# Kernel optimization log

Measured on AMD Instinct MI355X. Metric: run time of the kernel, lower is better.

Reference implementation:

```python
import jax, jax.numpy as jnp
import numpy as np

B, T, D, H = 2, 1024, 1024, 16
HS = D // H
EPS = 1e-5
SCALE = float(np.sqrt(HS))  # faithful bug: scores / hs**(-0.5) == scores * sqrt(hs)


def setup_inputs() -> dict:
    key = jax.random.key(0)
    ks = jax.random.split(key, 20)
    n = lambda k, shape: jax.random.normal(k, shape, dtype=jnp.float32) * 0.02
    return {
        "src": jax.random.normal(ks[0], (B, T, D), dtype=jnp.float32),
        "att": jax.random.normal(ks[1], (B, T, D), dtype=jnp.float32),
        # causal masked self-attention (no biases on q/k/v)
        "wq_m": n(ks[2], (H, D, HS)), "wk_m": n(ks[3], (H, D, HS)), "wv_m": n(ks[4], (H, D, HS)),
        "proj_m_w": n(ks[5], (D, D)), "proj_m_b": jnp.zeros((D,), jnp.float32),
        # final (cross) attention (biases on q/k/v)
        "wq_f": n(ks[6], (H, D, HS)), "wk_f": n(ks[7], (H, D, HS)), "wv_f": n(ks[8], (H, D, HS)),
        "bq_f": jnp.zeros((H, HS), jnp.float32), "bk_f": jnp.zeros((H, HS), jnp.float32),
        "bv_f": jnp.zeros((H, HS), jnp.float32),
        "proj_f_w": n(ks[9], (D, D)), "proj_f_b": jnp.zeros((D,), jnp.float32),
        # FFN
        "w1": n(ks[10], (D, 4 * D)), "b1": jnp.zeros((4 * D,), jnp.float32),
        "w2": n(ks[11], (4 * D, D)), "b2": jnp.zeros((D,), jnp.float32),
        # shared RMSNorm weight (one instance reused at all three sites)
        "norm_w": jnp.ones((D,), jnp.float32),
    }


def rmsnorm(x, w):
    return x * jax.lax.rsqrt(jnp.mean(x * x, axis=-1, keepdims=True) + EPS) * w


def masked_attn(x, wq, wk, wv):
    q = jnp.einsum('btd,hde->bhte', x, wq)
    k = jnp.einsum('btd,hde->bhte', x, wk)
    v = jnp.einsum('btd,hde->bhte', x, wv)
    scores = jnp.einsum('bhte,bhse->bhts', q, k) * SCALE  # [B,H,T,T]
    causal = jnp.tril(jnp.ones((T, T), dtype=bool))
    scores = jnp.where(causal, scores, -jnp.inf)
    a = jax.nn.softmax(scores, axis=-1)
    o = jnp.einsum('bhts,bhse->bhte', a, v)
    return o.transpose(0, 2, 1, 3).reshape(B, T, D)  # concat heads


def final_attn(x, att, wq, bq, wk, bk, wv, bv):
    q = jnp.einsum('btd,hde->bhte', att, wq) + bq[None, :, None, :]
    k = jnp.einsum('btd,hde->bhte', att, wk) + bk[None, :, None, :]
    v = jnp.einsum('btd,hde->bhte', x, wv) + bv[None, :, None, :]
    scores = jnp.einsum('bhte,bhse->bhts', q, k) * SCALE
    a = jax.nn.softmax(scores, axis=-1)
    o = jnp.einsum('bhts,bhse->bhte', a, v)
    return o.transpose(0, 2, 1, 3).reshape(B, T, D)


def reference(src, att, wq_m, wk_m, wv_m, proj_m_w, proj_m_b,
              wq_f, wk_f, wv_f, bq_f, bk_f, bv_f, proj_f_w, proj_f_b,
              w1, b1, w2, b2, norm_w):
    # masked self-attention block
    m = masked_attn(rmsnorm(src, norm_w), wq_m, wk_m, wv_m)
    m_out = src + (m @ proj_m_w + proj_m_b)
    # cross attention block (q/k from norm(att), v from m_out)
    f = final_attn(m_out, rmsnorm(att, norm_w), wq_f, bq_f, wk_f, bk_f, wv_f, bv_f)
    f_out = m_out + (f @ proj_f_w + proj_f_b)
    # FFN block
    h = rmsnorm(f_out, norm_w)
    h = jax.nn.gelu(h @ w1 + b1, approximate=False) @ w2 + b2
    return f_out + h
```

## Files before the change

### kernel.cpp

```cpp
#include <hip/hip_runtime.h>
#include <math.h>

#define BB 2
#define TT 1024
#define DD 1024
#define HH 16
#define HS 64
#define NROWS (BB*TT)

typedef _Float16 f16;
typedef __attribute__((ext_vector_type(8))) _Float16 half8;
typedef __attribute__((ext_vector_type(4))) _Float16 half4;
typedef __attribute__((ext_vector_type(4))) float f32x4;

constexpr float EPS   = 1e-5f;
constexpr float SCALE = 8.0f;

__device__ __forceinline__ void load_lds16(const f16* g, f16* l) {
    __builtin_amdgcn_global_load_lds(
        (const __attribute__((address_space(1))) unsigned int*)g,
        (__attribute__((address_space(3))) unsigned int*)l, 16, 0, 0);
}

__device__ __forceinline__ int xcd_swizzle(int lin, int total) {
    if ((total & 7) == 0) {
        const int chunk = total >> 3;
        lin = (lin & 7) * chunk + (lin >> 3);
    }
    return lin;
}

__global__ __launch_bounds__(256) void rmsnorm_kernel(const float* __restrict__ x,
                                                      const float* __restrict__ w,
                                                      f16* __restrict__ out) {
    const int row = blockIdx.x;
    const int tid = threadIdx.x;
    const float* xr = x + (size_t)row * DD;

    float4 xv = reinterpret_cast<const float4*>(xr)[tid];
    float ss = xv.x*xv.x + xv.y*xv.y + xv.z*xv.z + xv.w*xv.w;

    __shared__ float red[256];
    red[tid] = ss; __syncthreads();
    for (int s = 128; s > 0; s >>= 1) {
        if (tid < s) red[tid] += red[tid + s];
        __syncthreads();
    }
    const float inv = rsqrtf(red[0] * (1.0f / DD) + EPS);

    float4 wv = reinterpret_cast<const float4*>(w)[tid];
    half4 o;
    o.x = (f16)(xv.x * inv * wv.x);
    o.y = (f16)(xv.y * inv * wv.y);
    o.z = (f16)(xv.z * inv * wv.z);
    o.w = (f16)(xv.w * inv * wv.w);
    *reinterpret_cast<half4*>(&out[(size_t)row * DD + tid * 4]) = o;
}

template<bool HEADW>
__global__ __launch_bounds__(256) void wtrans(const float* __restrict__ W,
                                              f16* __restrict__ Wt,
                                              int K, int N) {
    __shared__ float t[64][65];
    const int k0 = blockIdx.x * 64;
    const int n0 = blockIdx.y * 64;
    const int tid = threadIdx.x;

    #pragma unroll
    for (int r = 0; r < 4; ++r) {
        const int idx = tid + r * 256;
        const int kl  = idx >> 4;
        const int nl4 = (idx & 15) * 4;
        const float* gp;
        if (HEADW) {
            gp = W + ((size_t)(n0 >> 6) * K + (k0 + kl)) * 64 + nl4;
        } else {
            gp = W + (size_t)(k0 + kl) * N + n0 + nl4;
        }
        float4 v = *reinterpret_cast<const float4*>(gp);
        t[kl][nl4 + 0] = v.x; t[kl][nl4 + 1] = v.y;
        t[kl][nl4 + 2] = v.z; t[kl][nl4 + 3] = v.w;
    }
    __syncthreads();
    #pragma unroll
    for (int r = 0; r < 4; ++r) {
        const int idx = tid + r * 256;
        const int nl  = idx >> 4;
        const int kl4 = (idx & 15) * 4;
        half4 o;
        o.x = (f16)t[kl4 + 0][nl];
        o.y = (f16)t[kl4 + 1][nl];
        o.z = (f16)t[kl4 + 2][nl];
        o.w = (f16)t[kl4 + 3][nl];
        *reinterpret_cast<half4*>(&Wt[(size_t)(n0 + nl) * K + k0 + kl4]) = o;
    }
}

__global__ void pack_bias(const float* __restrict__ a, const float* __restrict__ b,
                          const float* __restrict__ c, float* __restrict__ o) {
    const int i = blockIdx.x * 256 + threadIdx.x;
    if (i < 1024) { o[i] = a[i]; o[i + 1024] = b[i]; o[i + 2048] = c[i]; }
}

template<int BM, int EPI, bool HEADOUT, bool SPLITA, bool OHALF, bool OUT2, bool PARTIAL>
__global__ __launch_bounds__(256, 2) void gemm_mfma(
    const f16* __restrict__ A1,
    const f16* __restrict__ A2,
    const f16* __restrict__ Bt,
    const float* __restrict__ bias,
    const float* __restrict__ resid,
    float* __restrict__ outF,
    f16* __restrict__ outH,
    f16* __restrict__ outH2,
    int N, int K, int splitN)
{
    constexpr int BK = 32;
    constexpr int MI = 4;
    constexpr int NI = (BM == 128) ? 4 : 2;
    constexpr int WN = (BM == 128) ? 64 : 32;
    constexpr int ASLOT = BM * 4;
    constexpr int AINST = ASLOT / 256;

    __shared__ f16 ldsA[2][ASLOT * 8];
    __shared__ f16 ldsB[2][512 * 8];

    const int tid  = threadIdx.x;
    const int lane = tid & 63;
    const int wid  = tid >> 6;
    const int gx = gridDim.x;
    const int lin = xcd_swizzle(blockIdx.y * gx + blockIdx.x, gx * gridDim.y);
    const int m0 = (lin / gx) * BM;
    const int n0 = (lin % gx) * 128;
    const int wm = (BM == 128) ? (wid >> 1) : 0;
    const int wn = (BM == 128) ? (wid & 1) : wid;

    const int Klen  = K / gridDim.z;
    const int kbase = blockIdx.z * Klen;

    const f16* Aptr = (SPLITA && n0 >= splitN) ? A2 : A1;

    f32x4 acc[MI][NI];
    #pragma unroll
    for (int i = 0; i < MI; ++i)
        #pragma unroll
        for (int j = 0; j < NI; ++j)
            acc[i][j] = (f32x4){0.f, 0.f, 0.f, 0.f};

    auto stage = [&](int buf, int kt) {
        const int k0 = kbase + kt * BK;
        #pragma unroll
        for (int i = 0; i < AINST; ++i) {
            const int s   = (wid * AINST + i) * 64 + lane;
            const int kh  = s / BM;
            const int row = s % BM;
            load_lds16(Aptr + (size_t)(m0 + row) * K + (k0 + kh * 8),
                       &ldsA[buf][s * 8]);
        }
        #pragma unroll
        for (int i = 0; i < 2; ++i) {
            const int s   = (wid * 2 + i) * 64 + lane;
            const int kh  = s >> 7;
            const int col = s & 127;
            load_lds16(Bt + (size_t)(n0 + col) * K + (k0 + kh * 8),
                       &ldsB[buf][s * 8]);
        }
    };

    const int NT = Klen / BK;
    stage(0, 0);
    __syncthreads();
    int cur = 0;
    const int l15 = lane & 15, l4 = lane >> 4;
    for (int kt = 0; kt < NT; ++kt) {
        if (kt + 1 < NT) stage(cur ^ 1, kt + 1);
        half8 af[MI], bfr[NI];
        #pragma unroll
        for (int mi = 0; mi < MI; ++mi)
            af[mi] = *reinterpret_cast<const half8*>(
                &ldsA[cur][(l4 * BM + wm * 64 + mi * 16 + l15) * 8]);
        #pragma unroll
        for (int ni = 0; ni < NI; ++ni)
            bfr[ni] = *reinterpret_cast<const half8*>(
                &ldsB[cur][(l4 * 128 + wn * WN + ni * 16 + l15) * 8]);
        #pragma unroll
        for (int mi = 0; mi < MI; ++mi)
            #pragma unroll
            for (int ni = 0; ni < NI; ++ni)
                acc[mi][ni] = __builtin_amdgcn_mfma_f32_16x16x32_f16(
                    af[mi], bfr[ni], acc[mi][ni], 0, 0, 0);
        __syncthreads();
        cur ^= 1;
    }

    float* pout = nullptr;
    if (PARTIAL) {
        const size_t MN = (size_t)gridDim.y * BM * N;
        pout = outF + (size_t)blockIdx.z * MN;
    }

    #pragma unroll
    for (int mi = 0; mi < MI; ++mi) {
        #pragma unroll
        for (int ni = 0; ni < NI; ++ni) {
            #pragma unroll
            for (int r = 0; r < 4; ++r) {
                const int row = m0 + wm * 64 + mi * 16 + l4 * 4 + r;
                const int col = n0 + wn * WN + ni * 16 + l15;
                float v = acc[mi][ni][r];
                if (PARTIAL) {
                    pout[(size_t)row * N + col] = v;
                    continue;
                }
                if (EPI >= 1) v += bias[col];
                if (EPI == 2) v = 0.5f * v * (1.0f + erff(v * 0.70710678118f));
                if (EPI == 3) v += resid[(size_t)row * N + col];
                size_t oidx;
                if (HEADOUT) {
                    const int mat = col >> 10;
                    const int h = (col >> 6) & 15, e = col & 63;
                    const int b = row >> 10, t = row & (TT - 1);
                    oidx = (size_t)mat * ((size_t)NROWS * DD)
                         + ((size_t)((b * HH + h) * TT + t)) * HS + e;
                } else {
                    oidx = (size_t)row * N + col;
                }
                if (OHALF) outH[oidx] = (f16)v;
                else       outF[oidx] = v;
                if (OUT2)  outH2[oidx] = (f16)v;
            }
        }
    }
}

template<bool OUT2>
__global__ __launch_bounds__(256) void reduce4(const float* __restrict__ part,
                                               const float* __restrict__ bias,
                                               const float* __restrict__ resid,
                                               float* __restrict__ outF,
                                               f16* __restrict__ outH2,
                                               int N) {
    const size_t MN  = (size_t)gridDim.x * 1024;
    const size_t idx = ((size_t)blockIdx.x * 256 + threadIdx.x) * 4;
    float4 a = *reinterpret_cast<const float4*>(part + idx);
    float4 b = *reinterpret_cast<const float4*>(part + MN + idx);
    float4 c = *reinterpret_cast<const float4*>(part + 2 * MN + idx);
    float4 d = *reinterpret_cast<const float4*>(part + 3 * MN + idx);
    float4 bi = *reinterpret_cast<const float4*>(bias + (idx & (size_t)(N - 1)));
    float4 rs = *reinterpret_cast<const float4*>(resid + idx);
    float4 o;
    o.x = a.x + b.x + c.x + d.x + bi.x + rs.x;
    o.y = a.y + b.y + c.y + d.y + bi.y + rs.y;
    o.z = a.z + b.z + c.z + d.z + bi.z + rs.z;
    o.w = a.w + b.w + c.w + d.w + bi.w + rs.w;
    *reinterpret_cast<float4*>(outF + idx) = o;
    if (OUT2) {
        half4 h;
        h.x = (f16)o.x; h.y = (f16)o.y; h.z = (f16)o.z; h.w = (f16)o.w;
        *reinterpret_cast<half4*>(outH2 + idx) = h;
    }
}

template<bool CAUSAL>
__global__ __launch_bounds__(256) void attn_mfma(const f16* __restrict__ Q,
                                                 const f16* __restrict__ Kg,
                                                 const f16* __restrict__ Vg,
                                                 f16* __restrict__ O) {
    const int iq  = blockIdx.x;
    const int bh  = blockIdx.y;
    const int tid = threadIdx.x;
    const int lane = tid & 63;
    const int w   = tid >> 6;
    const int l15 = lane & 15, l4 = lane >> 4;

    __shared__ f16 Ks[512 * 8];
    __shared__ f16 VT[64 * 72];
    __shared__ f16 Ps[4][16 * 72];

    const f16* qb = Q  + ((size_t)bh * TT + (size_t)iq * 64) * HS;
    const f16* kb = Kg + (size_t)bh * TT * HS;
    const f16* vb = Vg + (size_t)bh * TT * HS;

    half8 qf[2];
    #pragma unroll
    for (int ks = 0; ks < 2; ++ks)
        qf[ks] = *reinterpret_cast<const half8*>(
            qb + (size_t)(w * 16 + l15) * HS + ks * 32 + l4 * 8);

    f32x4 oacc[4];
    #pragma unroll
    for (int ni = 0; ni < 4; ++ni) oacc[ni] = (f32x4){0.f, 0.f, 0.f, 0.f};
    float m_run[4], l_run[4];
    #pragma unroll
    for (int r = 0; r < 4; ++r) { m_run[r] = -1e30f; l_run[r] = 0.f; }

    const int sp  = lane & 31;
    const int ehv = lane >> 5;
    const int c0  = w * 16 + ehv * 8;

    const int ntiles = CAUSAL ? (iq + 1) : (TT / 64);
    for (int js = 0; js < ntiles; ++js) {
        __syncthreads();

        #pragma unroll
        for (int i = 0; i < 2; ++i) {
            const int slot = (w * 2 + i) * 64 + lane;
            load_lds16(kb + (size_t)(js * 64 + (slot & 63)) * HS + (slot >> 6) * 8,
                       &Ks[slot * 8]);
        }
        {
            const f16* vrow = vb + (size_t)(js * 64 + 2 * sp) * HS + c0;
            uint4 r0 = *reinterpret_cast<const uint4*>(vrow);
            uint4 r1 = *reinterpret_cast<const uint4*>(vrow + HS);
            const unsigned rc0[4] = {r0.x, r0.y, r0.z, r0.w};
            const unsigned rc1[4] = {r1.x, r1.y, r1.z, r1.w};
            #pragma unroll
            for (int i = 0; i < 8; ++i) {
                const unsigned lo = (i & 1) ? (rc0[i >> 1] >> 16) : (rc0[i >> 1] & 0xffffu);
                const unsigned hi = (i & 1) ? (rc1[i >> 1] >> 16) : (rc1[i >> 1] & 0xffffu);
                *reinterpret_cast<unsigned*>(&VT[(c0 + i) * 72 + 2 * sp]) = lo | (hi << 16);
            }
        }
        __syncthreads();

        f32x4 sacc[4];
        #pragma unroll
        for (int ni = 0; ni < 4; ++ni) sacc[ni] = (f32x4){0.f, 0.f, 0.f, 0.f};
        #pragma unroll
        for (int ks = 0; ks < 2; ++ks) {
            #pragma unroll
            for (int ni = 0; ni < 4; ++ni) {
                half8 kf = *reinterpret_cast<const half8*>(
                    &Ks[((ks * 4 + l4) * 64 + ni * 16 + l15) * 8]);
                sacc[ni] = __builtin_amdgcn_mfma_f32_16x16x32_f16(qf[ks], kf, sacc[ni], 0, 0, 0);
            }
        }

        float sv[4][4];
        #pragma unroll
        for (int ni = 0; ni < 4; ++ni) {
            #pragma unroll
            for (int r = 0; r < 4; ++r) {
                float x = sacc[ni][r] * SCALE;
                if (CAUSAL && js == iq) {
                    const int sg = js * 64 + ni * 16 + l15;
                    const int qg = iq * 64 + w * 16 + l4 * 4 + r;
                    if (sg > qg) x = -1e30f;
                }
                sv[ni][r] = x;
            }
        }

        #pragma unroll
        for (int r = 0; r < 4; ++r) {
            float rm = fmaxf(fmaxf(sv[0][r], sv[1][r]), fmaxf(sv[2][r], sv[3][r]));
            rm = fmaxf(rm, __shfl_xor(rm, 1));
            rm = fmaxf(rm, __shfl_xor(rm, 2));
            rm = fmaxf(rm, __shfl_xor(rm, 4));
            rm = fmaxf(rm, __shfl_xor(rm, 8));
            const float mnew = fmaxf(m_run[r], rm);
            const float corr = __expf(m_run[r] - mnew);
            float p0 = __expf(sv[0][r] - mnew);
            float p1 = __expf(sv[1][r] - mnew);
            float p2 = __expf(sv[2][r] - mnew);
            float p3 = __expf(sv[3][r] - mnew);
            float sum = p0 + p1 + p2 + p3;
            sum += __shfl_xor(sum, 1);
            sum += __shfl_xor(sum, 2);
            sum += __shfl_xor(sum, 4);
            sum += __shfl_xor(sum, 8);
            l_run[r] = l_run[r] * corr + sum;
            m_run[r] = mnew;
            #pragma unroll
            for (int ni = 0; ni < 4; ++ni) oacc[ni][r] *= corr;
            f16* prow = &Ps[w][(l4 * 4 + r) * 72];
            prow[ 0 + l15] = (f16)p0;
            prow[16 + l15] = (f16)p1;
            prow[32 + l15] = (f16)p2;
            prow[48 + l15] = (f16)p3;
        }

        #pragma unroll
        for (int ks = 0; ks < 2; ++ks) {
            half8 pf = *reinterpret_cast<const half8*>(&Ps[w][l15 * 72 + ks * 32 + l4 * 8]);
            #pragma unroll
            for (int ni = 0; ni < 4; ++ni) {
                half8 vf = *reinterpret_cast<const half8*>(
                    &VT[(ni * 16 + l15) * 72 + ks * 32 + l4 * 8]);
                oacc[ni] = __builtin_amdgcn_mfma_f32_16x16x32_f16(pf, vf, oacc[ni], 0, 0, 0);
            }
        }
    }

    const int b = bh >> 4, h = bh & (HH - 1);
    #pragma unroll
    for (int r = 0; r < 4; ++r) {
        const float inv = 1.0f / l_run[r];
        const int t = iq * 64 + w * 16 + l4 * 4 + r;
        #pragma unroll
        for (int ni = 0; ni < 4; ++ni)
            O[((size_t)(b * TT + t)) * DD + h * HS + ni * 16 + l15] =
                (f16)(oacc[ni][r] * inv);
    }
}

extern "C" void kernel_launch(void* const* d_in, const int* in_sizes, int n_in,
                              void* d_out, int out_size, void* d_ws, size_t ws_size,
                              hipStream_t stream) {
    const float* src      = (const float*)d_in[0];
    const float* att      = (const float*)d_in[1];
    const float* wq_m     = (const float*)d_in[2];
    const float* wk_m     = (const float*)d_in[3];
    const float* wv_m     = (const float*)d_in[4];
    const float* proj_m_w = (const float*)d_in[5];
    const float* proj_m_b = (const float*)d_in[6];
    const float* wq_f     = (const float*)d_in[7];
    const float* wk_f     = (const float*)d_in[8];
    const float* wv_f     = (const float*)d_in[9];
    const float* bq_f     = (const float*)d_in[10];
    const float* bk_f     = (const float*)d_in[11];
    const float* bv_f     = (const float*)d_in[12];
    const float* proj_f_w = (const float*)d_in[13];
    const float* proj_f_b = (const float*)d_in[14];
    const float* w1       = (const float*)d_in[15];
    const float* b1       = (const float*)d_in[16];
    const float* w2       = (const float*)d_in[17];
    const float* b2       = (const float*)d_in[18];
    const float* norm_w   = (const float*)d_in[19];

    const size_t M_ = 1024 * 1024;
    f16* wsb = (f16*)d_ws;
    f16* wt_qkvm = wsb;
    f16* wt_projm = wsb + 3 * M_;
    f16* wt_qkvf = wsb + 4 * M_;
    f16* wt_projf = wsb + 7 * M_;
    f16* wt_w1   = wsb + 8 * M_;
    f16* wt_w2   = wsb + 12 * M_;
    f16* xn  = wsb + 16 * M_;
    f16* qkv = wsb + 18 * M_;
    f16* ao  = wsb + 24 * M_;
    f16* h1  = wsb + 18 * M_;
    float* m_out = (float*)(wsb + 26 * M_);
    float* partb = (float*)(wsb + 30 * M_);
    f16* mo_h  = (f16*)d_out;
    float* biascat = (float*)((char*)d_out + 4 * 1024 * 1024);
    float* f_out = (float*)d_out;
    float* outp  = (float*)d_out;
    (void)ws_size; (void)in_sizes; (void)n_in;

    const dim3 blk(256);
    const int BIG = 1 << 30;
    const dim3 gSPLIT(8, 16, 4);
    const dim3 gRED(2048);

    pack_bias<<<dim3(4), blk, 0, stream>>>(bq_f, bk_f, bv_f, biascat);
    wtrans<true ><<<dim3(16, 16), blk, 0, stream>>>(wq_m, wt_qkvm + 0 * M_, 1024, 1024);
    wtrans<true ><<<dim3(16, 16), blk, 0, stream>>>(wk_m, wt_qkvm + 1 * M_, 1024, 1024);
    wtrans<true ><<<dim3(16, 16), blk, 0, stream>>>(wv_m, wt_qkvm + 2 * M_, 1024, 1024);
    wtrans<false><<<dim3(16, 16), blk, 0, stream>>>(proj_m_w, wt_projm, 1024, 1024);
    wtrans<true ><<<dim3(16, 16), blk, 0, stream>>>(wq_f, wt_qkvf + 0 * M_, 1024, 1024);
    wtrans<true ><<<dim3(16, 16), blk, 0, stream>>>(wk_f, wt_qkvf + 1 * M_, 1024, 1024);
    wtrans<true ><<<dim3(16, 16), blk, 0, stream>>>(wv_f, wt_qkvf + 2 * M_, 1024, 1024);
    wtrans<false><<<dim3(16, 16), blk, 0, stream>>>(proj_f_w, wt_projf, 1024, 1024);
    wtrans<false><<<dim3(16, 64), blk, 0, stream>>>(w1, wt_w1, 1024, 4096);
    wtrans<false><<<dim3(64, 16), blk, 0, stream>>>(w2, wt_w2, 4096, 1024);

    rmsnorm_kernel<<<dim3(NROWS), blk, 0, stream>>>(src, norm_w, xn);
    gemm_mfma<128, 0, true, false, true, false, false><<<dim3(24, 16), blk, 0, stream>>>(
        xn, nullptr, wt_qkvm, nullptr, nullptr, nullptr, qkv, nullptr, 3072, 1024, BIG);
    attn_mfma<true><<<dim3(16, 32), blk, 0, stream>>>(qkv, qkv + 2 * M_, qkv + 4 * M_, ao);
    gemm_mfma<128, 0, false, false, false, false, true><<<gSPLIT, blk, 0, stream>>>(
        ao, nullptr, wt_projm, nullptr, nullptr, partb, nullptr, nullptr, 1024, 1024, BIG);
    reduce4<true><<<gRED, blk, 0, stream>>>(partb, proj_m_b, src, m_out, mo_h, 1024);

    rmsnorm_kernel<<<dim3(NROWS), blk, 0, stream>>>(att, norm_w, xn);
    gemm_mfma<128, 1, true, true, true, false, false><<<dim3(24, 16), blk, 0, stream>>>(
        xn, mo_h, wt_qkvf, biascat, nullptr, nullptr, qkv, nullptr, 3072, 1024, 2048);
    attn_mfma<false><<<dim3(16, 32), blk, 0, stream>>>(qkv, qkv + 2 * M_, qkv + 4 * M_, ao);
    gemm_mfma<128, 0, false, false, false, false, true><<<gSPLIT, blk, 0, stream>>>(
        ao, nullptr, wt_projf, nullptr, nullptr, partb, nullptr, nullptr, 1024, 1024, BIG);
    reduce4<false><<<gRED, blk, 0, stream>>>(partb, proj_f_b, m_out, f_out, nullptr, 1024);

    rmsnorm_kernel<<<dim3(NROWS), blk, 0, stream>>>(f_out, norm_w, xn);
    gemm_mfma<128, 2, false, false, true, false, false><<<dim3(32, 16), blk, 0, stream>>>(
        xn, nullptr, wt_w1, b1, nullptr, nullptr, h1, nullptr, 4096, 1024, BIG);
    gemm_mfma<128, 0, false, false, false, false, true><<<gSPLIT, blk, 0, stream>>>(
        h1, nullptr, wt_w2, nullptr, nullptr, partb, nullptr, nullptr, 1024, 4096, BIG);
    reduce4<false><<<gRED, blk, 0, stream>>>(partb, b2, f_out, outp, nullptr, 1024);
}
```

Measured before the change: 339.0 us.

## Merge weight transposes into one launch, shrink GEMM M-tile, reorder block mapping

Folds the ten weight-transpose launches and the bias pack into a single wtrans_all kernel that dispatches on block index, cutting launch overhead. All GEMMs switch from 128-row to 64-row tiles with doubled grid rows, giving more blocks for better CU occupancy and tail balance. The linear block index is now mapped column-major (m fastest), so consecutive blocks share B-tiles. Smaller tiles lower per-block data reuse and increase global traffic.

```diff
diff --git a/kernel.cpp b/kernel.cpp
--- a/kernel.cpp
+++ b/kernel.cpp
@@ -57,29 +57,67 @@
     *reinterpret_cast<half4*>(&out[(size_t)row * DD + tid * 4]) = o;
 }
 
-template<bool HEADW>
-__global__ __launch_bounds__(256) void wtrans(const float* __restrict__ W,
-                                              f16* __restrict__ Wt,
-                                              int K, int N) {
-    __shared__ float t[64][65];
-    const int k0 = blockIdx.x * 64;
-    const int n0 = blockIdx.y * 64;
+__global__ __launch_bounds__(256) void wtrans_all(
+    const float* __restrict__ wq_m, const float* __restrict__ wk_m,
+    const float* __restrict__ wv_m, const float* __restrict__ proj_m_w,
+    const float* __restrict__ wq_f, const float* __restrict__ wk_f,
+    const float* __restrict__ wv_f, const float* __restrict__ proj_f_w,
+    const float* __restrict__ w1,   const float* __restrict__ w2,
+    f16* __restrict__ d_qkvm, f16* __restrict__ d_projm,
+    f16* __restrict__ d_qkvf, f16* __restrict__ d_projf,
+    f16* __restrict__ d_w1,   f16* __restrict__ d_w2,
+    const float* __restrict__ bq, const float* __restrict__ bk,
+    const float* __restrict__ bv, float* __restrict__ biascat)
+{
+    const int bid = blockIdx.x;
     const int tid = threadIdx.x;
-
+    const size_t M_ = 1024 * 1024;
+
+    if (bid >= 4096) {
+        #pragma unroll
+        for (int r = 0; r < 4; ++r) {
+            const int j = r * 256 + tid;
+            biascat[j] = bq[j]; biascat[j + 1024] = bk[j]; biascat[j + 2048] = bv[j];
+        }
+        return;
+    }
+
+    const float* W; f16* Wt; int K, N, lognk, t; bool headw;
+    if (bid < 768)       { const int m = bid >> 8;
+                           W = (m == 0) ? wq_m : (m == 1) ? wk_m : wv_m;
+                           Wt = d_qkvm + (size_t)m * M_;
+                           K = 1024; N = 1024; lognk = 4; headw = true;  t = bid & 255; }
+    else if (bid < 1024) { W = proj_m_w; Wt = d_projm;
+                           K = 1024; N = 1024; lognk = 4; headw = false; t = bid - 768; }
+    else if (bid < 1792) { const int m = (bid - 1024) >> 8;
+                           W = (m == 0) ? wq_f : (m == 1) ? wk_f : wv_f;
+                           Wt = d_qkvf + (size_t)m * M_;
+                           K = 1024; N = 1024; lognk = 4; headw = true;  t = (bid - 1024) & 255; }
+    else if (bid < 2048) { W = proj_f_w; Wt = d_projf;
+                           K = 1024; N = 1024; lognk = 4; headw = false; t = bid - 1792; }
+    else if (bid < 3072) { W = w1; Wt = d_w1;
+                           K = 1024; N = 4096; lognk = 4; headw = false; t = bid - 2048; }
+    else                 { W = w2; Wt = d_w2;
+                           K = 4096; N = 1024; lognk = 6; headw = false; t = bid - 3072; }
+
+    const int k0 = (t & ((1 << lognk) - 1)) * 64;
+    const int n0 = (t >> lognk) * 64;
+
+    __shared__ float tt[64][65];
     #pragma unroll
     for (int r = 0; r < 4; ++r) {
         const int idx = tid + r * 256;
         const int kl  = idx >> 4;
         const int nl4 = (idx & 15) * 4;
         const float* gp;
-        if (HEADW) {
+        if (headw) {
             gp = W + ((size_t)(n0 >> 6) * K + (k0 + kl)) * 64 + nl4;
         } else {
             gp = W + (size_t)(k0 + kl) * N + n0 + nl4;
         }
         float4 v = *reinterpret_cast<const float4*>(gp);
-        t[kl][nl4 + 0] = v.x; t[kl][nl4 + 1] = v.y;
-        t[kl][nl4 + 2] = v.z; t[kl][nl4 + 3] = v.w;
+        tt[kl][nl4 + 0] = v.x; tt[kl][nl4 + 1] = v.y;
+        tt[kl][nl4 + 2] = v.z; tt[kl][nl4 + 3] = v.w;
     }
     __syncthreads();
     #pragma unroll
@@ -88,18 +126,12 @@
         const int nl  = idx >> 4;
         const int kl4 = (idx & 15) * 4;
         half4 o;
-        o.x = (f16)t[kl4 + 0][nl];
-        o.y = (f16)t[kl4 + 1][nl];
-        o.z = (f16)t[kl4 + 2][nl];
-        o.w = (f16)t[kl4 + 3][nl];
+        o.x = (f16)tt[kl4 + 0][nl];
+        o.y = (f16)tt[kl4 + 1][nl];
+        o.z = (f16)tt[kl4 + 2][nl];
+        o.w = (f16)tt[kl4 + 3][nl];
         *reinterpret_cast<half4*>(&Wt[(size_t)(n0 + nl) * K + k0 + kl4]) = o;
     }
-}
-
-__global__ void pack_bias(const float* __restrict__ a, const float* __restrict__ b,
-                          const float* __restrict__ c, float* __restrict__ o) {
-    const int i = blockIdx.x * 256 + threadIdx.x;
-    if (i < 1024) { o[i] = a[i]; o[i + 1024] = b[i]; o[i + 2048] = c[i]; }
 }
 
 template<int BM, int EPI, bool HEADOUT, bool SPLITA, bool OHALF, bool OUT2, bool PARTIAL>
@@ -127,10 +159,11 @@
     const int tid  = threadIdx.x;
     const int lane = tid & 63;
     const int wid  = tid >> 6;
-    const int gx = gridDim.x;
-    const int lin = xcd_swizzle(blockIdx.y * gx + blockIdx.x, gx * gridDim.y);
-    const int m0 = (lin / gx) * BM;
-    const int n0 = (lin % gx) * 128;
+    const int gy = gridDim.y;
+    const int lin = xcd_swizzle(blockIdx.y * gridDim.x + blockIdx.x,
+                                gridDim.x * gy);
+    const int m0 = (lin % gy) * BM;
+    const int n0 = (lin / gy) * 128;
     const int wm = (BM == 128) ? (wid >> 1) : 0;
     const int wn = (BM == 128) ? (wid & 1) : wid;
 
@@ -449,41 +482,36 @@
 
     const dim3 blk(256);
     const int BIG = 1 << 30;
-    const dim3 gSPLIT(8, 16, 4);
+    const dim3 gQKV(24, 32);
+    const dim3 gW1(32, 32);
+    const dim3 gSPLIT(8, 32, 4);
     const dim3 gRED(2048);
 
-    pack_bias<<<dim3(4), blk, 0, stream>>>(bq_f, bk_f, bv_f, biascat);
-    wtrans<true ><<<dim3(16, 16), blk, 0, stream>>>(wq_m, wt_qkvm + 0 * M_, 1024, 1024);
-    wtrans<true ><<<dim3(16, 16), blk, 0, stream>>>(wk_m, wt_qkvm + 1 * M_, 1024, 1024);
-    wtrans<true ><<<dim3(16, 16), blk, 0, stream>>>(wv_m, wt_qkvm + 2 * M_, 1024, 1024);
-    wtrans<false><<<dim3(16, 16), blk, 0, stream>>>(proj_m_w, wt_projm, 1024, 1024);
-    wtrans<true ><<<dim3(16, 16), blk, 0, stream>>>(wq_f, wt_qkvf + 0 * M_, 1024, 1024);
-    wtrans<true ><<<dim3(16, 16), blk, 0, stream>>>(wk_f, wt_qkvf + 1 * M_, 1024, 1024);
-    wtrans<true ><<<dim3(16, 16), blk, 0, stream>>>(wv_f, wt_qkvf + 2 * M_, 1024, 1024);
-    wtrans<false><<<dim3(16, 16), blk, 0, stream>>>(proj_f_w, wt_projf, 1024, 1024);
-    wtrans<false><<<dim3(16, 64), blk, 0, stream>>>(w1, wt_w1, 1024, 4096);
-    wtrans<false><<<dim3(64, 16), blk, 0, stream>>>(w2, wt_w2, 4096, 1024);
+    wtrans_all<<<dim3(4097), blk, 0, stream>>>(
+        wq_m, wk_m, wv_m, proj_m_w, wq_f, wk_f, wv_f, proj_f_w, w1, w2,
+        wt_qkvm, wt_projm, wt_qkvf, wt_projf, wt_w1, wt_w2,
+        bq_f, bk_f, bv_f, biascat);
 
     rmsnorm_kernel<<<dim3(NROWS), blk, 0, stream>>>(src, norm_w, xn);
-    gemm_mfma<128, 0, true, false, true, false, false><<<dim3(24, 16), blk, 0, stream>>>(
+    gemm_mfma<64, 0, true, false, true, false, false><<<gQKV, blk, 0, stream>>>(
         xn, nullptr, wt_qkvm, nullptr, nullptr, nullptr, qkv, nullptr, 3072, 1024, BIG);
     attn_mfma<true><<<dim3(16, 32), blk, 0, stream>>>(qkv, qkv + 2 * M_, qkv + 4 * M_, ao);
-    gemm_mfma<128, 0, false, false, false, false, true><<<gSPLIT, blk, 0, stream>>>(
+    gemm_mfma<64, 0, false, false, false, false, true><<<gSPLIT, blk, 0, stream>>>(
         ao, nullptr, wt_projm, nullptr, nullptr, partb, nullptr, nullptr, 1024, 1024, BIG);
     reduce4<true><<<gRED, blk, 0, stream>>>(partb, proj_m_b, src, m_out, mo_h, 1024);
 
     rmsnorm_kernel<<<dim3(NROWS), blk, 0, stream>>>(att, norm_w, xn);
-    gemm_mfma<128, 1, true, true, true, false, false><<<dim3(24, 16), blk, 0, stream>>>(
+    gemm_mfma<64, 1, true, true, true, false, false><<<gQKV, blk, 0, stream>>>(
         xn, mo_h, wt_qkvf, biascat, nullptr, nullptr, qkv, nullptr, 3072, 1024, 2048);
     attn_mfma<false><<<dim3(16, 32), blk, 0, stream>>>(qkv, qkv + 2 * M_, qkv + 4 * M_, ao);
-    gemm_mfma<128, 0, false, false, false, false, true><<<gSPLIT, blk, 0, stream>>>(
+    gemm_mfma<64, 0, false, false, false, false, true><<<gSPLIT, blk, 0, stream>>>(
         ao, nullptr, wt_projf, nullptr, nullptr, partb, nullptr, nullptr, 1024, 1024, BIG);
     reduce4<false><<<gRED, blk, 0, stream>>>(partb, proj_f_b, m_out, f_out, nullptr, 1024);
 
     rmsnorm_kernel<<<dim3(NROWS), blk, 0, stream>>>(f_out, norm_w, xn);
-    gemm_mfma<128, 2, false, false, true, false, false><<<dim3(32, 16), blk, 0, stream>>>(
+    gemm_mfma<64, 2, false, false, true, false, false><<<gW1, blk, 0, stream>>>(
         xn, nullptr, wt_w1, b1, nullptr, nullptr, h1, nullptr, 4096, 1024, BIG);
-    gemm_mfma<128, 0, false, false, false, false, true><<<gSPLIT, blk, 0, stream>>>(
+    gemm_mfma<64, 0, false, false, false, false, true><<<gSPLIT, blk, 0, stream>>>(
         h1, nullptr, wt_w2, nullptr, nullptr, partb, nullptr, nullptr, 1024, 4096, BIG);
     reduce4<false><<<gRED, blk, 0, stream>>>(partb, b2, f_out, outp, nullptr, 1024);
 }
```

Measured after the change: 364.5 us. 1.08x slower.
